# Performance work log

Measured on AMD Instinct MI355X. Metric: run time of the kernel, lower is better.

The kernel has to match this reference:

```python
import jax, jax.numpy as jnp
import numpy as np

# config constants
B, L, ENC_IN = 8, 512, 7
D_MODEL = 768
EXPAND = 2
D_INNER = D_MODEL * EXPAND          # 1536
DT_RANK = (D_MODEL + 15) // 16      # 48
N_STATE = 16                         # configs.d_ff acts as SSM state size
K_CONV = 4
E_LAYERS = 2
C_OUT = 7
PRED_LEN = 96
EPS = 1e-5


def rmsnorm(x, w):
    return x * jax.lax.rsqrt(jnp.mean(x * x, axis=-1, keepdims=True) + EPS) * w


def silu(x):
    return x * jax.nn.sigmoid(x)


def positional_embedding(l, d):
    pos = np.arange(l, dtype=np.float32)[:, None]
    div = np.exp(np.arange(0, d, 2, dtype=np.float32) * (-np.log(10000.0) / d))
    pe = np.zeros((l, d), dtype=np.float32)
    pe[:, 0::2] = np.sin(pos * div)
    pe[:, 1::2] = np.cos(pos * div)
    return jnp.asarray(pe)


def causal_dwconv(x, w, b):
    # x: [b, d, l], w: [d, 1, k]; torch pads k-1 both sides then slices [:l] == left-pad k-1
    y = jax.lax.conv_general_dilated(
        x, w, window_strides=(1,), padding=[(K_CONV - 1, 0)],
        dimension_numbers=('NCH', 'OIH', 'NCH'), feature_group_count=D_INNER)
    return y + b[None, :, None]


def selective_scan(u, delta, A, Bm, Cm, Dp):
    # u, delta: [b,l,d]; A: [d,n]; Bm, Cm: [b,l,n]; Dp: [d]
    deltaA = jnp.exp(jnp.einsum('bld,dn->bldn', delta, A))          # [b,l,d,n]
    deltaBu = (delta * u)[..., None] * Bm[:, :, None, :]             # [b,l,d,n]

    def step(xc, inp):
        dA, dBu, Ct = inp                                            # [b,d,n],[b,d,n],[b,n]
        xc = dA * xc + dBu
        return xc, jnp.einsum('bdn,bn->bd', xc, Ct)

    b, l, d = u.shape
    x0 = jnp.zeros((b, d, A.shape[1]), u.dtype)
    _, ys = jax.lax.scan(step, x0, (jnp.moveaxis(deltaA, 1, 0),
                                    jnp.moveaxis(deltaBu, 1, 0),
                                    jnp.moveaxis(Cm, 1, 0)))
    y = jnp.moveaxis(ys, 0, 1)                                       # [b,l,d]
    return y + u * Dp


def mamba_block(x, in_w, conv_w, conv_b, xproj_w, dtproj_w, dtproj_b, A_log, Dp, outproj_w):
    xr = x @ in_w.T                                                  # [b,l,2*d_inner]
    xs, res = xr[..., :D_INNER], xr[..., D_INNER:]
    xs = causal_dwconv(jnp.swapaxes(xs, 1, 2), conv_w, conv_b)
    xs = silu(jnp.swapaxes(xs, 1, 2))
    # ssm
    A = -jnp.exp(A_log)
    x_dbl = xs @ xproj_w.T                                           # [b,l,dt_rank+2n]
    delta = x_dbl[..., :DT_RANK]
    Bm = x_dbl[..., DT_RANK:DT_RANK + N_STATE]
    Cm = x_dbl[..., DT_RANK + N_STATE:]
    delta = jax.nn.softplus(delta @ dtproj_w.T + dtproj_b)
    y = selective_scan(xs, delta, A, Bm, Cm, Dp)
    y = y * silu(res)
    return y @ outproj_w.T


def setup_inputs() -> dict:
    key = jax.random.key(0)
    ks = iter(jax.random.split(key, 32))
    s = 0.02
    d = {}
    d['x'] = jax.random.normal(next(ks), (B, L, ENC_IN), jnp.float32)
    d['token_w'] = jax.random.normal(next(ks), (D_MODEL, ENC_IN, 3), jnp.float32) * s
    d['time_w'] = jax.random.normal(next(ks), (D_MODEL, 1), jnp.float32) * s
    d['norm_w'] = jnp.ones((E_LAYERS, D_MODEL), jnp.float32)
    d['in_w'] = jax.random.normal(next(ks), (E_LAYERS, 2 * D_INNER, D_MODEL), jnp.float32) * s
    d['conv_w'] = jax.random.normal(next(ks), (E_LAYERS, D_INNER, 1, K_CONV), jnp.float32) * s
    d['conv_b'] = jnp.zeros((E_LAYERS, D_INNER), jnp.float32)
    d['xproj_w'] = jax.random.normal(next(ks), (E_LAYERS, DT_RANK + 2 * N_STATE, D_INNER), jnp.float32) * s
    d['dtproj_w'] = jax.random.normal(next(ks), (E_LAYERS, D_INNER, DT_RANK), jnp.float32) * s
    d['dtproj_b'] = jnp.zeros((E_LAYERS, D_INNER), jnp.float32)
    A = np.tile(np.arange(1, N_STATE + 1, dtype=np.float32)[None, :], (D_INNER, 1))
    d['A_log'] = jnp.tile(jnp.log(jnp.asarray(A))[None], (E_LAYERS, 1, 1))
    d['Dp'] = jnp.ones((E_LAYERS, D_INNER), jnp.float32)
    d['outproj_w'] = jax.random.normal(next(ks), (E_LAYERS, D_MODEL, D_INNER), jnp.float32) * s
    d['final_norm_w'] = jnp.ones((D_MODEL,), jnp.float32)
    d['out_w'] = jax.random.normal(next(ks), (C_OUT, D_MODEL), jnp.float32) * s
    return d


def reference(x, token_w, time_w, norm_w, in_w, conv_w, conv_b, xproj_w,
              dtproj_w, dtproj_b, A_log, Dp, outproj_w, final_norm_w, out_w):
    # instance normalization (mean/std detached)
    mean_enc = jax.lax.stop_gradient(jnp.mean(x, axis=1, keepdims=True))
    xc = x - mean_enc
    std_enc = jax.lax.stop_gradient(jnp.sqrt(jnp.var(xc, axis=1, keepdims=True) + 1e-5))
    xc = xc / std_enc
    # DataEmbedding: circular conv token emb + sinusoidal pos + timeF linear
    xp = jnp.pad(jnp.swapaxes(xc, 1, 2), ((0, 0), (0, 0), (1, 1)), mode='wrap')
    tok = jax.lax.conv_general_dilated(xp, token_w, (1,), 'VALID',
                                       dimension_numbers=('NCH', 'OIH', 'NCH'))
    tok = jnp.swapaxes(tok, 1, 2)                                    # [b,l,d_model]
    x_mark = (jnp.arange(L, dtype=x.dtype) / L)[None, :, None]       # [1,l,1]
    h = tok + positional_embedding(L, D_MODEL)[None] + x_mark @ time_w.T
    for e in range(E_LAYERS):
        h = mamba_block(rmsnorm(h, norm_w[e]), in_w[e], conv_w[e], conv_b[e],
                        xproj_w[e], dtproj_w[e], dtproj_b[e], A_log[e], Dp[e],
                        outproj_w[e]) + h
    h = rmsnorm(h, final_norm_w)
    out = h @ out_w.T
    out = out * std_enc + mean_enc
    return out[:, -PRED_LEN:, :]
```

## Files before the change

kernel.cpp:

```cpp
#include <hip/hip_runtime.h>
#include <hip/hip_bf16.h>
#include <math.h>

#define BSZ 8
#define LSEQ 512
#define ENC_IN 7
#define D_MODEL 768
#define D_INNER 1536
#define DT_RANK 48
#define N_STATE 16
#define K_CONV 4
#define E_LAYERS 2
#define C_OUT 7
#define PRED_LEN 96
#define EPSV 1e-5f
#define XN 80
#define KSPLIT 4

#define ROWS (BSZ*LSEQ)
#define NC 16
#define CL (LSEQ/NC)
#define NTILE (LSEQ/16)
#define LOG2E 1.44269504088896f

typedef __bf16 bf16x8 __attribute__((ext_vector_type(8)));
typedef float  f32x4  __attribute__((ext_vector_type(4)));

__device__ __forceinline__ float fexp2(float x) {
    float r;
    asm("v_exp_f32 %0, %1" : "=v"(r) : "v"(x));
    return r;
}
__device__ __forceinline__ float softplusf(float v) {
    return fmaxf(v, 0.f) + log1pf(__expf(-fabsf(v)));
}

__device__ __forceinline__ float block_sum(float v, float* tmp) {
    #pragma unroll
    for (int off = 32; off > 0; off >>= 1) v += __shfl_down(v, off);
    int lane = threadIdx.x & 63, wid = threadIdx.x >> 6;
    __syncthreads();
    if (lane == 0) tmp[wid] = v;
    __syncthreads();
    return tmp[0] + tmp[1] + tmp[2] + tmp[3];
}

__global__ __launch_bounds__(256) void cvt_all(const float* __restrict__ in_w,
                                               const float* __restrict__ outw,
                                               const float* __restrict__ xpw,
                                               const float* __restrict__ dtw,
                                               __hip_bfloat16* __restrict__ inw_bf,
                                               __hip_bfloat16* __restrict__ outw_bf,
                                               __hip_bfloat16* __restrict__ xpw_bf,
                                               __hip_bfloat16* __restrict__ dtw_bf) {
    const int N1 = E_LAYERS*2*D_INNER*D_MODEL;
    const int N2 = E_LAYERS*D_MODEL*D_INNER;
    const int N3 = E_LAYERS*XN*D_INNER;
    const int N4 = E_LAYERS*D_INNER*64;
    int i = blockIdx.x*256 + threadIdx.x;
    if (i < N1) {
        inw_bf[i] = __float2bfloat16(in_w[i]);
    } else if (i < N1+N2) {
        int j = i - N1; outw_bf[j] = __float2bfloat16(outw[j]);
    } else if (i < N1+N2+N3) {
        int j = i - N1 - N2; xpw_bf[j] = __float2bfloat16(xpw[j]);
    } else if (i < N1+N2+N3+N4) {
        int j = i - N1 - N2 - N3;
        int r = j >> 6, c = j & 63;
        dtw_bf[j] = __float2bfloat16(c < DT_RANK ? dtw[r*DT_RANK + c] : 0.f);
    }
}

__global__ __launch_bounds__(256) void stats_kernel(const float* __restrict__ x,
                                                    float* __restrict__ mean,
                                                    float* __restrict__ stdv) {
    int bc = blockIdx.x;
    int b = bc / ENC_IN, c = bc % ENC_IN;
    __shared__ float tmp[4];
    float s = 0.f, sq = 0.f;
    for (int l = threadIdx.x; l < LSEQ; l += 256) {
        float v = x[((size_t)(b*LSEQ + l))*ENC_IN + c];
        s += v; sq += v*v;
    }
    s = block_sum(s, tmp);
    sq = block_sum(sq, tmp);
    if (threadIdx.x == 0) {
        float m = s / LSEQ;
        float var = sq / LSEQ - m*m;
        if (var < 0.f) var = 0.f;
        mean[bc] = m;
        stdv[bc] = sqrtf(var + EPSV);
    }
}

__global__ __launch_bounds__(256) void embed_kernel(const float* __restrict__ x,
                                                    const float* __restrict__ token_w,
                                                    const float* __restrict__ time_w,
                                                    const float* __restrict__ mean,
                                                    const float* __restrict__ stdv,
                                                    float* __restrict__ h) {
    int bl = blockIdx.x;
    int b = bl >> 9, l = bl & 511;
    __shared__ float sxc[ENC_IN*3];
    if (threadIdx.x < ENC_IN*3) {
        int c = threadIdx.x / 3, k = threadIdx.x % 3;
        int lk = (l + k - 1) & 511;
        float v = x[((size_t)(b*LSEQ + lk))*ENC_IN + c];
        sxc[threadIdx.x] = (v - mean[b*ENC_IN + c]) / stdv[b*ENC_IN + c];
    }
    __syncthreads();
    #pragma unroll
    for (int i = 0; i < 3; i++) {
        int d = threadIdx.x + i*256;
        float acc = 0.f;
        const float* w = token_w + (size_t)d*21;
        #pragma unroll
        for (int t = 0; t < 21; t++) acc += sxc[t] * w[t];
        int d2 = d & ~1;
        float div = __expf((float)d2 * (-9.210340371976184f / (float)D_MODEL));
        float ang = (float)l * div;
        float pe = (d & 1) ? cosf(ang) : sinf(ang);
        float tm = ((float)l / (float)LSEQ) * time_w[d];
        h[(size_t)bl*D_MODEL + d] = acc + pe + tm;
    }
}

__global__ __launch_bounds__(256) void rmsnorm_bf16(const float* __restrict__ h,
                                                    const float* __restrict__ w,
                                                    __hip_bfloat16* __restrict__ xn) {
    size_t base = (size_t)blockIdx.x * D_MODEL;
    __shared__ float tmp[4];
    float ss = 0.f;
    for (int k = threadIdx.x; k < D_MODEL; k += 256) { float v = h[base+k]; ss += v*v; }
    ss = block_sum(ss, tmp);
    float inv = rsqrtf(ss / (float)D_MODEL + EPSV);
    for (int k = threadIdx.x; k < D_MODEL; k += 256)
        xn[base+k] = __float2bfloat16(h[base+k]*inv*w[k]);
}

__global__ __launch_bounds__(256) void gemm_inproj(const __hip_bfloat16* __restrict__ A,
                                                   const __hip_bfloat16* __restrict__ Bw,
                                                   __hip_bfloat16* __restrict__ Cxs,
                                                   __hip_bfloat16* __restrict__ Cg) {
    __shared__ __align__(16) __hip_bfloat16 As[128*64];
    __shared__ __align__(16) __hip_bfloat16 Bs[128*64];
    const int K = D_MODEL;
    int tid = threadIdx.x, lane = tid & 63, w = tid >> 6;
    int gx = gridDim.x;
    int nwg = gx * gridDim.y;
    int orig = blockIdx.y*gx + blockIdx.x;
    int swz = (orig & 7)*(nwg >> 3) + (orig >> 3);
    int m0 = (swz / gx) * 128, n0 = (swz % gx) * 128;
    int wr = w >> 1, wc = w & 1;
    int kq = lane >> 4, rr = lane & 15;

    f32x4 acc[4][4];
    #pragma unroll
    for (int i = 0; i < 4; i++)
        #pragma unroll
        for (int j = 0; j < 4; j++) acc[i][j] = (f32x4){0.f,0.f,0.f,0.f};

    const char* Ab = (const char*)A;
    const char* Bb = (const char*)Bw;
    char* AsB = (char*)As;
    char* BsB = (char*)Bs;

    for (int k0 = 0; k0 < K; k0 += 64) {
        #pragma unroll
        for (int c = 0; c < 4; c++) {
            int idx = c*256 + tid;
            int r = idx >> 3, q = idx & 7;
            int qs = q ^ (r & 7);
            __builtin_amdgcn_global_load_lds(
                (const __attribute__((address_space(1))) unsigned int*)(Ab + ((size_t)(m0+r)*K + k0 + qs*8)*2),
                (__attribute__((address_space(3))) unsigned int*)(AsB + idx*16), 16, 0, 0);
            __builtin_amdgcn_global_load_lds(
                (const __attribute__((address_space(1))) unsigned int*)(Bb + ((size_t)(n0+r)*K + k0 + qs*8)*2),
                (__attribute__((address_space(3))) unsigned int*)(BsB + idx*16), 16, 0, 0);
        }
        __syncthreads();

        #pragma unroll
        for (int kh = 0; kh < 2; kh++) {
            int ch = ((kh*4 + kq) ^ (rr & 7)) * 16;
            bf16x8 af[4], bfr[4];
            #pragma unroll
            for (int mi = 0; mi < 4; mi++) af[mi]  = *(const bf16x8*)(AsB + (wr*64 + mi*16 + rr)*128 + ch);
            #pragma unroll
            for (int ni = 0; ni < 4; ni++) bfr[ni] = *(const bf16x8*)(BsB + (wc*64 + ni*16 + rr)*128 + ch);
            #pragma unroll
            for (int mi = 0; mi < 4; mi++)
                #pragma unroll
                for (int ni = 0; ni < 4; ni++)
                    acc[mi][ni] = __builtin_amdgcn_mfma_f32_16x16x32_bf16(af[mi], bfr[ni], acc[mi][ni], 0, 0, 0);
        }
        __syncthreads();
    }

    #pragma unroll
    for (int mi = 0; mi < 4; mi++) {
        #pragma unroll
        for (int ni = 0; ni < 4; ni++) {
            int row0 = m0 + wr*64 + mi*16;
            int col  = n0 + wc*64 + ni*16 + rr;
            if (col >= D_INNER) {
                __hip_bfloat16 g4[4];
                #pragma unroll
                for (int r = 0; r < 4; r++) {
                    float v = acc[mi][ni][r];
                    g4[r] = __float2bfloat16(v / (1.f + __expf(-v)));
                }
                int cd = col - D_INNER;
                *(uint2*)&Cg[((size_t)(row0 >> 4)*D_INNER + cd)*16 + kq*4] = *(uint2*)g4;
            } else {
                #pragma unroll
                for (int r = 0; r < 4; r++) {
                    int row = row0 + kq*4 + r;
                    Cxs[(size_t)row*D_INNER + col] = __float2bfloat16(acc[mi][ni][r]);
                }
            }
        }
    }
}

__global__ __launch_bounds__(256) void gemm_dtproj(const __hip_bfloat16* __restrict__ A,
                                                   const __hip_bfloat16* __restrict__ Bw,
                                                   const float* __restrict__ bias,
                                                   float* __restrict__ C) {
    __shared__ __align__(16) __hip_bfloat16 As[128*64];
    __shared__ __align__(16) __hip_bfloat16 Bs[128*64];
    const int K = 64;
    int tid = threadIdx.x, lane = tid & 63, w = tid >> 6;
    int gx = gridDim.x;
    int nwg = gx * gridDim.y;
    int orig = blockIdx.y*gx + blockIdx.x;
    int swz = (orig & 7)*(nwg >> 3) + (orig >> 3);
    int m0 = (swz / gx) * 128, n0 = (swz % gx) * 128;
    int wr = w >> 1, wc = w & 1;
    int kq = lane >> 4, rr = lane & 15;

    f32x4 acc[4][4];
    #pragma unroll
    for (int i = 0; i < 4; i++)
        #pragma unroll
        for (int j = 0; j < 4; j++) acc[i][j] = (f32x4){0.f,0.f,0.f,0.f};

    const char* Ab = (const char*)A;
    const char* Bb = (const char*)Bw;
    char* AsB = (char*)As;
    char* BsB = (char*)Bs;

    #pragma unroll
    for (int c = 0; c < 4; c++) {
        int idx = c*256 + tid;
        int r = idx >> 3, q = idx & 7;
        int qs = q ^ (r & 7);
        __builtin_amdgcn_global_load_lds(
            (const __attribute__((address_space(1))) unsigned int*)(Ab + ((size_t)(m0+r)*K + qs*8)*2),
            (__attribute__((address_space(3))) unsigned int*)(AsB + idx*16), 16, 0, 0);
        __builtin_amdgcn_global_load_lds(
            (const __attribute__((address_space(1))) unsigned int*)(Bb + ((size_t)(n0+r)*K + qs*8)*2),
            (__attribute__((address_space(3))) unsigned int*)(BsB + idx*16), 16, 0, 0);
    }
    __syncthreads();

    #pragma unroll
    for (int kh = 0; kh < 2; kh++) {
        int ch = ((kh*4 + kq) ^ (rr & 7)) * 16;
        bf16x8 af[4], bfr[4];
        #pragma unroll
        for (int mi = 0; mi < 4; mi++) af[mi]  = *(const bf16x8*)(AsB + (wr*64 + mi*16 + rr)*128 + ch);
        #pragma unroll
        for (int ni = 0; ni < 4; ni++) bfr[ni] = *(const bf16x8*)(BsB + (wc*64 + ni*16 + rr)*128 + ch);
        #pragma unroll
        for (int mi = 0; mi < 4; mi++)
            #pragma unroll
            for (int ni = 0; ni < 4; ni++)
                acc[mi][ni] = __builtin_amdgcn_mfma_f32_16x16x32_bf16(af[mi], bfr[ni], acc[mi][ni], 0, 0, 0);
    }

    #pragma unroll
    for (int mi = 0; mi < 4; mi++) {
        #pragma unroll
        for (int ni = 0; ni < 4; ni++) {
            int row0 = m0 + wr*64 + mi*16;
            int col  = n0 + wc*64 + ni*16 + rr;
            float4 v4;
            #pragma unroll
            for (int r = 0; r < 4; r++) {
                float v = acc[mi][ni][r] + bias[col];
                ((float*)&v4)[r] = softplusf(v);
            }
            *(float4*)&C[((size_t)(row0 >> 4)*D_INNER + col)*16 + kq*4] = v4;
        }
    }
}

__global__ __launch_bounds__(256) void gemm_outproj(const __hip_bfloat16* __restrict__ A,
                                                    const __hip_bfloat16* __restrict__ Bw,
                                                    float* __restrict__ C) {
    __shared__ __align__(16) __hip_bfloat16 As[128*32];
    __shared__ __align__(16) __hip_bfloat16 Bs[64*32];
    int tid = threadIdx.x, lane = tid & 63, w = tid >> 6;
    int gx = gridDim.x;
    int nwg = gx * gridDim.y;
    int orig = blockIdx.y*gx + blockIdx.x;
    int swz = (orig & 7)*(nwg >> 3) + (orig >> 3);
    int m0 = (swz / gx) * 128, n0 = (swz % gx) * 64;
    int wr = w >> 1, wc = w & 1;
    int kq = lane >> 4, rr = lane & 15;
    const int K = D_INNER;

    f32x4 acc[4][2];
    #pragma unroll
    for (int i = 0; i < 4; i++)
        #pragma unroll
        for (int j = 0; j < 2; j++) acc[i][j] = (f32x4){0.f,0.f,0.f,0.f};

    const char* Ab = (const char*)A;
    const char* Bb = (const char*)Bw;
    char* AsB = (char*)As;
    char* BsB = (char*)Bs;

    int cA0 = tid, cA1 = tid + 256;
    int rA0 = cA0 >> 2, qA0 = (cA0 & 3) ^ ((rA0 >> 1) & 3);
    int rA1 = cA1 >> 2, qA1 = (cA1 & 3) ^ ((rA1 >> 1) & 3);
    int rB = tid >> 2,  qB  = (tid & 3) ^ ((rB >> 1) & 3);
    int sw = (kq ^ ((rr >> 1) & 3)) * 16;

    for (int k0 = 0; k0 < K; k0 += 32) {
        __builtin_amdgcn_global_load_lds(
            (const __attribute__((address_space(1))) unsigned int*)(Ab + ((size_t)(m0+rA0)*K + k0 + qA0*8)*2),
            (__attribute__((address_space(3))) unsigned int*)(AsB + cA0*16), 16, 0, 0);
        __builtin_amdgcn_global_load_lds(
            (const __attribute__((address_space(1))) unsigned int*)(Ab + ((size_t)(m0+rA1)*K + k0 + qA1*8)*2),
            (__attribute__((address_space(3))) unsigned int*)(AsB + cA1*16), 16, 0, 0);
        __builtin_amdgcn_global_load_lds(
            (const __attribute__((address_space(1))) unsigned int*)(Bb + ((size_t)(n0+rB)*K + k0 + qB*8)*2),
            (__attribute__((address_space(3))) unsigned int*)(BsB + tid*16), 16, 0, 0);
        __syncthreads();

        bf16x8 af[4], bfr[2];
        #pragma unroll
        for (int mi = 0; mi < 4; mi++) af[mi]  = *(const bf16x8*)(AsB + (wr*64 + mi*16 + rr)*64 + sw);
        #pragma unroll
        for (int ni = 0; ni < 2; ni++) bfr[ni] = *(const bf16x8*)(BsB + (wc*32 + ni*16 + rr)*64 + sw);
        #pragma unroll
        for (int mi = 0; mi < 4; mi++)
            #pragma unroll
            for (int ni = 0; ni < 2; ni++)
                acc[mi][ni] = __builtin_amdgcn_mfma_f32_16x16x32_bf16(af[mi], bfr[ni], acc[mi][ni], 0, 0, 0);
        __syncthreads();
    }

    #pragma unroll
    for (int mi = 0; mi < 4; mi++) {
        #pragma unroll
        for (int ni = 0; ni < 2; ni++) {
            #pragma unroll
            for (int r = 0; r < 4; r++) {
                int row = m0 + wr*64 + mi*16 + kq*4 + r;
                int col = n0 + wc*32 + ni*16 + rr;
                size_t o = (size_t)row*D_MODEL + col;
                C[o] = acc[mi][ni][r] + C[o];
            }
        }
    }
}

__global__ __launch_bounds__(256) void gemm_xproj(const __hip_bfloat16* __restrict__ A,
                                                  const __hip_bfloat16* __restrict__ W,
                                                  float* __restrict__ P) {
    __shared__ __align__(16) __hip_bfloat16 As[64*64];
    __shared__ __align__(16) __hip_bfloat16 Bs[96*64];
    int tid = threadIdx.x, lane = tid & 63, w = tid >> 6;
    int m0 = blockIdx.x * 64;
    int k0 = blockIdx.y * (D_INNER / KSPLIT);
    int kq = lane >> 4, rr = lane & 15;
    f32x4 acc[5];
    #pragma unroll
    for (int i = 0; i < 5; i++) acc[i] = (f32x4){0.f,0.f,0.f,0.f};
    const char* Ab = (const char*)A;
    const char* Wb = (const char*)W;
    char* AsB = (char*)As;
    char* BsB = (char*)Bs;

    for (int kk = k0; kk < k0 + D_INNER/KSPLIT; kk += 64) {
        #pragma unroll
        for (int cA = 0; cA < 2; cA++) {
            int idx = cA*256 + tid;
            int r = idx >> 3, q = (idx & 7) ^ (r & 7);
            __builtin_amdgcn_global_load_lds(
                (const __attribute__((address_space(1))) unsigned int*)(Ab + ((size_t)(m0+r)*D_INNER + kk + q*8)*2),
                (__attribute__((address_space(3))) unsigned int*)(AsB + idx*16), 16, 0, 0);
        }
        #pragma unroll
        for (int cB = 0; cB < 3; cB++) {
            int idx = cB*256 + tid;
            int r = idx >> 3, q = (idx & 7) ^ (r & 7);
            int rs = r < XN ? r : XN-1;
            __builtin_amdgcn_global_load_lds(
                (const __attribute__((address_space(1))) unsigned int*)(Wb + ((size_t)rs*D_INNER + kk + q*8)*2),
                (__attribute__((address_space(3))) unsigned int*)(BsB + idx*16), 16, 0, 0);
        }
        __syncthreads();
        #pragma unroll
        for (int kh = 0; kh < 2; kh++) {
            bf16x8 a = *(const bf16x8*)(AsB + (w*16 + rr)*128 + (((kh*4 + kq) ^ (rr & 7)))*16);
            #pragma unroll
            for (int ni = 0; ni < 5; ni++) {
                bf16x8 b = *(const bf16x8*)(BsB + (ni*16 + rr)*128 + (((kh*4 + kq) ^ (rr & 7)))*16);
                acc[ni] = __builtin_amdgcn_mfma_f32_16x16x32_bf16(a, b, acc[ni], 0, 0, 0);
            }
        }
        __syncthreads();
    }
    float* Cp = P + (size_t)blockIdx.y * ROWS * XN;
    #pragma unroll
    for (int ni = 0; ni < 5; ni++)
        #pragma unroll
        for (int r = 0; r < 4; r++) {
            int row = m0 + w*16 + kq*4 + r;
            int col = ni*16 + rr;
            Cp[(size_t)row*XN + col] = acc[ni][r];
        }
}

__global__ __launch_bounds__(256) void xproj_reduce(const float* __restrict__ P,
                                                    float* __restrict__ xdbl,
                                                    __hip_bfloat16* __restrict__ xdbl_bf) {
    int idx = blockIdx.x*256 + threadIdx.x;
    int col = idx % 96, row = idx / 96;
    if (row >= ROWS) return;
    const size_t RX = (size_t)ROWS*XN;
    if (col < XN) {
        size_t o = (size_t)row*XN + col;
        float s = P[o] + P[RX + o] + P[2*RX + o] + P[3*RX + o];
        xdbl[o] = s;
        if (col < DT_RANK) xdbl_bf[(size_t)row*64 + col] = __float2bfloat16(s);
    } else {
        xdbl_bf[(size_t)row*64 + col - 32] = __float2bfloat16(0.f);
    }
}

__global__ __launch_bounds__(256) void dwconv_silu(const __hip_bfloat16* __restrict__ xs,
                                                   const float* __restrict__ cw,
                                                   const float* __restrict__ cb,
                                                   __hip_bfloat16* __restrict__ u_bf) {
    int idx = blockIdx.x*256 + threadIdx.x;
    int dg = idx % (D_INNER/8);
    int t  = idx / (D_INNER/8);
    if (t >= ROWS) return;
    int d0 = dg*8;
    int l = t & 511, b = t >> 9;
    bf16x8 rows[K_CONV];
    #pragma unroll
    for (int k = 0; k < K_CONV; k++) {
        int ll = l - (K_CONV-1) + k;
        if (ll >= 0) rows[k] = *(const bf16x8*)(xs + ((size_t)(b*LSEQ + ll))*D_INNER + d0);
        else { bf16x8 z = {}; rows[k] = z; }
    }
    bf16x8 outv;
    #pragma unroll
    for (int j = 0; j < 8; j++) {
        int d = d0 + j;
        const float4 w4 = *(const float4*)(cw + d*K_CONV);
        float acc = cb[d]
                  + (float)rows[0][j]*w4.x + (float)rows[1][j]*w4.y
                  + (float)rows[2][j]*w4.z + (float)rows[3][j]*w4.w;
        float v = acc / (1.f + __expf(-acc));
        outv[j] = (__bf16)v;
    }
    *(bf16x8*)(u_bf + (size_t)t*D_INNER + d0) = outv;
}

__global__ __launch_bounds__(256) void scan_p1(const __hip_bfloat16* __restrict__ u,
                                               const float* __restrict__ delta_blk,
                                               const float* __restrict__ xdbl,
                                               const float* __restrict__ A_log,
                                               float* __restrict__ xfin,
                                               float* __restrict__ sumdlt) {
    int d = blockIdx.x*256 + threadIdx.x;
    int c = blockIdx.y, b = blockIdx.z;
    int l0 = c*CL;
    float A2[N_STATE], xs[N_STATE];
    const float* al = A_log + d*N_STATE;
    #pragma unroll
    for (int n = 0; n < N_STATE; n++) {
        A2[n] = -__expf(al[n]) * LOG2E;
        xs[n] = 0.f;
    }
    const __hip_bfloat16* pu = u + (size_t)(b*LSEQ + l0)*D_INNER + d;
    const float* pB = xdbl + (size_t)(b*LSEQ + l0)*XN + DT_RANK;
    float sd = 0.f;
    #pragma unroll
    for (int tt = 0; tt < 2; tt++) {
        const float* db = delta_blk + ((size_t)(b*NTILE + (l0>>4) + tt)*D_INNER + d)*16;
        float dl[16];
        #pragma unroll
        for (int q = 0; q < 4; q++) {
            f32x4 v = *(const f32x4*)(db + q*4);
            dl[q*4+0]=v[0]; dl[q*4+1]=v[1]; dl[q*4+2]=v[2]; dl[q*4+3]=v[3];
        }
        #pragma unroll
        for (int i = 0; i < 16; i++) {
            float dlt = dl[i];
            float uu = __bfloat162float(*pu); pu += D_INNER;
            float du = dlt*uu;
            sd += dlt;
            #pragma unroll
            for (int n = 0; n < N_STATE; n++)
                xs[n] = fexp2(dlt*A2[n])*xs[n] + du*pB[n];
            pB += XN;
        }
    }
    float* px = xfin + (size_t)((b*NC + c)*N_STATE)*D_INNER + d;
    #pragma unroll
    for (int n = 0; n < N_STATE; n++) px[n*D_INNER] = xs[n];
    sumdlt[(size_t)(b*NC + c)*D_INNER + d] = sd;
}

__global__ __launch_bounds__(256) void scan_p2(float* __restrict__ xfin,
                                               const float* __restrict__ sumdlt,
                                               const float* __restrict__ A_log) {
    int idx = blockIdx.x*256 + threadIdx.x;
    int d = idx % D_INNER;
    int r = idx / D_INNER;
    int n = r & 15;
    int b = r >> 4;
    float A2 = -__expf(A_log[d*N_STATE + n]) * LOG2E;
    float cr = 0.f;
    for (int c = 1; c < NC; c++) {
        size_t jp = (size_t)(b*NC + c - 1);
        float xf = xfin[(jp*N_STATE + n)*D_INNER + d];
        float s  = sumdlt[jp*D_INNER + d];
        cr = fexp2(A2 * s) * cr + xf;
        xfin[(jp*N_STATE + n)*D_INNER + d] = cr;
    }
}

__global__ __launch_bounds__(256) void scan_p3(const __hip_bfloat16* __restrict__ u,
                                               const float* __restrict__ delta_blk,
                                               const __hip_bfloat16* __restrict__ gres,
                                               const float* __restrict__ xdbl,
                                               const float* __restrict__ A_log,
                                               const float* __restrict__ Dp,
                                               const float* __restrict__ carry,
                                               __hip_bfloat16* __restrict__ ygate) {
    int d = blockIdx.x*256 + threadIdx.x;
    int c = blockIdx.y, b = blockIdx.z;
    int l0 = c*CL;
    float A2[N_STATE], xs[N_STATE];
    const float* al = A_log + d*N_STATE;
    #pragma unroll
    for (int n = 0; n < N_STATE; n++) A2[n] = -__expf(al[n]) * LOG2E;
    if (c == 0) {
        #pragma unroll
        for (int n = 0; n < N_STATE; n++) xs[n] = 0.f;
    } else {
        const float* pc = carry + (size_t)((b*NC + c - 1)*N_STATE)*D_INNER + d;
        #pragma unroll
        for (int n = 0; n < N_STATE; n++) xs[n] = pc[n*D_INNER];
    }
    float Dv = Dp[d];
    const __hip_bfloat16* pu = u + (size_t)(b*LSEQ + l0)*D_INNER + d;
    const float* pB = xdbl + (size_t)(b*LSEQ + l0)*XN + DT_RANK;
    __hip_bfloat16* py = ygate + (size_t)(b*LSEQ + l0)*D_INNER + d;
    #pragma unroll
    for (int tt = 0; tt < 2; tt++) {
        size_t tb = (size_t)(b*NTILE + (l0>>4) + tt)*D_INNER + d;
        const float* db = delta_blk + tb*16;
        float dl[16];
        #pragma unroll
        for (int q = 0; q < 4; q++) {
            f32x4 v = *(const f32x4*)(db + q*4);
            dl[q*4+0]=v[0]; dl[q*4+1]=v[1]; dl[q*4+2]=v[2]; dl[q*4+3]=v[3];
        }
        const __hip_bfloat16* gb = gres + tb*16;
        bf16x8 g0 = *(const bf16x8*)gb;
        bf16x8 g1 = *(const bf16x8*)(gb + 8);
        float gr[16];
        #pragma unroll
        for (int j = 0; j < 8; j++) { gr[j] = (float)g0[j]; gr[8+j] = (float)g1[j]; }
        #pragma unroll
        for (int i = 0; i < 16; i++) {
            float dlt = dl[i];
            float uu = __bfloat162float(*pu); pu += D_INNER;
            float du = dlt*uu;
            float acc = 0.f;
            #pragma unroll
            for (int n = 0; n < N_STATE; n++) {
                xs[n] = fexp2(dlt*A2[n])*xs[n] + du*pB[n];
                acc += xs[n]*pB[N_STATE + n];
            }
            pB += XN;
            float y = acc + uu*Dv;
            *py = __float2bfloat16(y * gr[i]); py += D_INNER;
        }
    }
}

__global__ __launch_bounds__(256) void final_kernel(const float* __restrict__ h,
                                                    const float* __restrict__ fnw,
                                                    const float* __restrict__ out_w,
                                                    const float* __restrict__ mean,
                                                    const float* __restrict__ stdv,
                                                    float* __restrict__ out) {
    int bid = blockIdx.x;
    int b = bid / PRED_LEN, lo = bid % PRED_LEN;
    int l = LSEQ - PRED_LEN + lo;
    const float* row = h + ((size_t)(b*LSEQ + l))*D_MODEL;
    __shared__ float tmp[4];
    float ss = 0.f;
    for (int k = threadIdx.x; k < D_MODEL; k += 256) { float v = row[k]; ss += v*v; }
    ss = block_sum(ss, tmp);
    float inv = rsqrtf(ss / (float)D_MODEL + EPSV);
    float acc[C_OUT] = {};
    for (int k = threadIdx.x; k < D_MODEL; k += 256) {
        float hn = row[k]*fnw[k];
        #pragma unroll
        for (int c = 0; c < C_OUT; c++) acc[c] += hn*out_w[c*D_MODEL + k];
    }
    #pragma unroll
    for (int c = 0; c < C_OUT; c++) {
        float s = block_sum(acc[c], tmp);
        if (threadIdx.x == 0)
            out[((size_t)(b*PRED_LEN + lo))*C_OUT + c] = s*inv*stdv[b*ENC_IN + c] + mean[b*ENC_IN + c];
    }
}

extern "C" void kernel_launch(void* const* d_in, const int* in_sizes, int n_in,
                              void* d_out, int out_size, void* d_ws, size_t ws_size,
                              hipStream_t stream) {
    const float* x        = (const float*)d_in[0];
    const float* token_w  = (const float*)d_in[1];
    const float* time_w   = (const float*)d_in[2];
    const float* norm_w   = (const float*)d_in[3];
    const float* in_w     = (const float*)d_in[4];
    const float* conv_w   = (const float*)d_in[5];
    const float* conv_b   = (const float*)d_in[6];
    const float* xproj_w  = (const float*)d_in[7];
    const float* dtproj_w = (const float*)d_in[8];
    const float* dtproj_b = (const float*)d_in[9];
    const float* A_log    = (const float*)d_in[10];
    const float* Dp       = (const float*)d_in[11];
    const float* outproj_w= (const float*)d_in[12];
    const float* final_nw = (const float*)d_in[13];
    const float* out_w    = (const float*)d_in[14];
    float* out = (float*)d_out;

    float* ws   = (float*)d_ws;
    float* mean = ws;
    float* stdv = ws + 64;
    float* h    = ws + 128;
    float* xdbl = h    + (size_t)ROWS*D_MODEL;
    float* delta= xdbl + (size_t)ROWS*XN;
    float* sumd = delta+ (size_t)ROWS*D_INNER;
    float* xfin = sumd + (size_t)BSZ*NC*D_INNER;
    float* pout = xfin + (size_t)BSZ*NC*D_INNER*N_STATE;
    float* fend = pout + (size_t)KSPLIT*ROWS*XN;
    __hip_bfloat16* xn_bf  = (__hip_bfloat16*)fend;
    __hip_bfloat16* xs_bf  = xn_bf + (size_t)ROWS*D_MODEL;
    __hip_bfloat16* u_bf   = xs_bf + (size_t)ROWS*D_INNER;
    __hip_bfloat16* gres   = u_bf  + (size_t)ROWS*D_INNER;
    __hip_bfloat16* ygate  = gres  + (size_t)ROWS*D_INNER;
    __hip_bfloat16* xdbl_bf= ygate + (size_t)ROWS*D_INNER;
    __hip_bfloat16* inw_bf = xdbl_bf+ (size_t)ROWS*64;
    __hip_bfloat16* outw_bf= inw_bf + (size_t)E_LAYERS*2*D_INNER*D_MODEL;
    __hip_bfloat16* xpw_bf = outw_bf+ (size_t)E_LAYERS*D_MODEL*D_INNER;
    __hip_bfloat16* dtw_bf = xpw_bf + (size_t)E_LAYERS*XN*D_INNER;

    {
        const int NT = E_LAYERS*2*D_INNER*D_MODEL + E_LAYERS*D_MODEL*D_INNER
                     + E_LAYERS*XN*D_INNER + E_LAYERS*D_INNER*64;
        cvt_all<<<(NT+255)/256, 256, 0, stream>>>(in_w, outproj_w, xproj_w, dtproj_w,
                                                  inw_bf, outw_bf, xpw_bf, dtw_bf);
    }

    stats_kernel<<<BSZ*ENC_IN, 256, 0, stream>>>(x, mean, stdv);
    embed_kernel<<<ROWS, 256, 0, stream>>>(x, token_w, time_w, mean, stdv, h);

    for (int e = 0; e < E_LAYERS; e++) {
        rmsnorm_bf16<<<ROWS, 256, 0, stream>>>(h, norm_w + e*D_MODEL, xn_bf);
        gemm_inproj<<<dim3(2*D_INNER/128, ROWS/128), 256, 0, stream>>>(
            xn_bf, inw_bf + (size_t)e*2*D_INNER*D_MODEL, xs_bf, gres);
        dwconv_silu<<<(ROWS*(D_INNER/8) + 255)/256, 256, 0, stream>>>(
            xs_bf, conv_w + (size_t)e*D_INNER*K_CONV, conv_b + e*D_INNER, u_bf);
        gemm_xproj<<<dim3(ROWS/64, KSPLIT), 256, 0, stream>>>(
            u_bf, xpw_bf + (size_t)e*XN*D_INNER, pout);
        xproj_reduce<<<(ROWS*96 + 255)/256, 256, 0, stream>>>(pout, xdbl, xdbl_bf);
        gemm_dtproj<<<dim3(D_INNER/128, ROWS/128), 256, 0, stream>>>(
            xdbl_bf, dtw_bf + (size_t)e*D_INNER*64, dtproj_b + e*D_INNER, delta);
        const float* Alog_e = A_log + (size_t)e*D_INNER*N_STATE;
        scan_p1<<<dim3(D_INNER/256, NC, BSZ), 256, 0, stream>>>(
            u_bf, delta, xdbl, Alog_e, xfin, sumd);
        scan_p2<<<(BSZ*D_INNER*N_STATE)/256, 256, 0, stream>>>(
            xfin, sumd, Alog_e);
        scan_p3<<<dim3(D_INNER/256, NC, BSZ), 256, 0, stream>>>(
            u_bf, delta, gres, xdbl, Alog_e, Dp + (size_t)e*D_INNER, xfin, ygate);
        gemm_outproj<<<dim3(D_MODEL/64, ROWS/128), 256, 0, stream>>>(
            ygate, outw_bf + (size_t)e*D_MODEL*D_INNER, h);
    }

    final_kernel<<<BSZ*PRED_LEN, 256, 0, stream>>>(h, final_nw, out_w, mean, stdv, out);
}
```

Baseline: 415.6 us.

## Double-buffer GEMM tiles, store delta as bf16, add power-chain scan fast path

The in_proj, out_proj and x_proj GEMMs now use two LDS buffers, so the next K slice is prefetched while MFMAs run on the current one. dt_proj writes softplus(delta) as bf16 instead of fp32, which halves that tensor's traffic in the two scan kernels. The scan kernels check at runtime whether exp(A_log[n]) equals n+1 (the standard Mamba initialisation). When it does, they replace the 16 per-step exponentials with one exp2 followed by repeated multiplication, and fall back to the general path otherwise. The costs are bf16 rounding of delta, small accumulated error from the power chain, and more LDS and register use in the GEMMs.

```diff
diff --git a/kernel.cpp b/kernel.cpp
--- a/kernel.cpp
+++ b/kernel.cpp
@@ -33,6 +33,10 @@
 }
 __device__ __forceinline__ float softplusf(float v) {
     return fmaxf(v, 0.f) + log1pf(__expf(-fabsf(v)));
+}
+__device__ __forceinline__ void glds16(const char* g, char* l) {
+    __builtin_amdgcn_global_load_lds((const __attribute__((address_space(1))) unsigned int*)g,
+                                     (__attribute__((address_space(3))) unsigned int*)l, 16, 0, 0);
 }
 
 __device__ __forceinline__ float block_sum(float v, float* tmp) {
@@ -142,8 +146,8 @@
                                                    const __hip_bfloat16* __restrict__ Bw,
                                                    __hip_bfloat16* __restrict__ Cxs,
                                                    __hip_bfloat16* __restrict__ Cg) {
-    __shared__ __align__(16) __hip_bfloat16 As[128*64];
-    __shared__ __align__(16) __hip_bfloat16 Bs[128*64];
+    __shared__ __align__(16) __hip_bfloat16 As[2][128*32];
+    __shared__ __align__(16) __hip_bfloat16 Bs[2][128*32];
     const int K = D_MODEL;
     int tid = threadIdx.x, lane = tid & 63, w = tid >> 6;
     int gx = gridDim.x;
@@ -165,36 +169,40 @@
     char* AsB = (char*)As;
     char* BsB = (char*)Bs;
 
-    for (int k0 = 0; k0 < K; k0 += 64) {
-        #pragma unroll
-        for (int c = 0; c < 4; c++) {
-            int idx = c*256 + tid;
-            int r = idx >> 3, q = idx & 7;
-            int qs = q ^ (r & 7);
-            __builtin_amdgcn_global_load_lds(
-                (const __attribute__((address_space(1))) unsigned int*)(Ab + ((size_t)(m0+r)*K + k0 + qs*8)*2),
-                (__attribute__((address_space(3))) unsigned int*)(AsB + idx*16), 16, 0, 0);
-            __builtin_amdgcn_global_load_lds(
-                (const __attribute__((address_space(1))) unsigned int*)(Bb + ((size_t)(n0+r)*K + k0 + qs*8)*2),
-                (__attribute__((address_space(3))) unsigned int*)(BsB + idx*16), 16, 0, 0);
-        }
+    int c0 = tid, c1 = tid + 256;
+    int r0 = c0 >> 2, q0 = (c0 & 3) ^ ((r0 >> 1) & 3);
+    int r1 = c1 >> 2, q1 = (c1 & 3) ^ ((r1 >> 1) & 3);
+    int sw = (kq ^ ((rr >> 1) & 3)) * 16;
+
+    glds16(Ab + ((size_t)(m0+r0)*K + 0 + q0*8)*2, AsB + c0*16);
+    glds16(Ab + ((size_t)(m0+r1)*K + 0 + q1*8)*2, AsB + c1*16);
+    glds16(Bb + ((size_t)(n0+r0)*K + 0 + q0*8)*2, BsB + c0*16);
+    glds16(Bb + ((size_t)(n0+r1)*K + 0 + q1*8)*2, BsB + c1*16);
+    asm volatile("s_waitcnt vmcnt(0)" ::: "memory");
+    __syncthreads();
+
+    int cur = 0;
+    for (int k0 = 0; k0 < K; k0 += 32) {
+        if (k0 + 32 < K) {
+            int nb = cur ^ 1;
+            glds16(Ab + ((size_t)(m0+r0)*K + k0+32 + q0*8)*2, AsB + nb*8192 + c0*16);
+            glds16(Ab + ((size_t)(m0+r1)*K + k0+32 + q1*8)*2, AsB + nb*8192 + c1*16);
+            glds16(Bb + ((size_t)(n0+r0)*K + k0+32 + q0*8)*2, BsB + nb*8192 + c0*16);
+            glds16(Bb + ((size_t)(n0+r1)*K + k0+32 + q1*8)*2, BsB + nb*8192 + c1*16);
+        }
+        bf16x8 af[4], bfr[4];
+        #pragma unroll
+        for (int mi = 0; mi < 4; mi++) af[mi]  = *(const bf16x8*)(AsB + cur*8192 + (wr*64 + mi*16 + rr)*64 + sw);
+        #pragma unroll
+        for (int ni = 0; ni < 4; ni++) bfr[ni] = *(const bf16x8*)(BsB + cur*8192 + (wc*64 + ni*16 + rr)*64 + sw);
+        #pragma unroll
+        for (int mi = 0; mi < 4; mi++)
+            #pragma unroll
+            for (int ni = 0; ni < 4; ni++)
+                acc[mi][ni] = __builtin_amdgcn_mfma_f32_16x16x32_bf16(af[mi], bfr[ni], acc[mi][ni], 0, 0, 0);
+        asm volatile("s_waitcnt vmcnt(0)" ::: "memory");
         __syncthreads();
-
-        #pragma unroll
-        for (int kh = 0; kh < 2; kh++) {
-            int ch = ((kh*4 + kq) ^ (rr & 7)) * 16;
-            bf16x8 af[4], bfr[4];
-            #pragma unroll
-            for (int mi = 0; mi < 4; mi++) af[mi]  = *(const bf16x8*)(AsB + (wr*64 + mi*16 + rr)*128 + ch);
-            #pragma unroll
-            for (int ni = 0; ni < 4; ni++) bfr[ni] = *(const bf16x8*)(BsB + (wc*64 + ni*16 + rr)*128 + ch);
-            #pragma unroll
-            for (int mi = 0; mi < 4; mi++)
-                #pragma unroll
-                for (int ni = 0; ni < 4; ni++)
-                    acc[mi][ni] = __builtin_amdgcn_mfma_f32_16x16x32_bf16(af[mi], bfr[ni], acc[mi][ni], 0, 0, 0);
-        }
-        __syncthreads();
+        cur ^= 1;
     }
 
     #pragma unroll
@@ -226,7 +234,7 @@
 __global__ __launch_bounds__(256) void gemm_dtproj(const __hip_bfloat16* __restrict__ A,
                                                    const __hip_bfloat16* __restrict__ Bw,
                                                    const float* __restrict__ bias,
-                                                   float* __restrict__ C) {
+                                                   __hip_bfloat16* __restrict__ C) {
     __shared__ __align__(16) __hip_bfloat16 As[128*64];
     __shared__ __align__(16) __hip_bfloat16 Bs[128*64];
     const int K = 64;
@@ -255,12 +263,8 @@
         int idx = c*256 + tid;
         int r = idx >> 3, q = idx & 7;
         int qs = q ^ (r & 7);
-        __builtin_amdgcn_global_load_lds(
-            (const __attribute__((address_space(1))) unsigned int*)(Ab + ((size_t)(m0+r)*K + qs*8)*2),
-            (__attribute__((address_space(3))) unsigned int*)(AsB + idx*16), 16, 0, 0);
-        __builtin_amdgcn_global_load_lds(
-            (const __attribute__((address_space(1))) unsigned int*)(Bb + ((size_t)(n0+r)*K + qs*8)*2),
-            (__attribute__((address_space(3))) unsigned int*)(BsB + idx*16), 16, 0, 0);
+        glds16(Ab + ((size_t)(m0+r)*K + qs*8)*2, AsB + idx*16);
+        glds16(Bb + ((size_t)(n0+r)*K + qs*8)*2, BsB + idx*16);
     }
     __syncthreads();
 
@@ -285,13 +289,13 @@
         for (int ni = 0; ni < 4; ni++) {
             int row0 = m0 + wr*64 + mi*16;
             int col  = n0 + wc*64 + ni*16 + rr;
-            float4 v4;
+            __hip_bfloat16 d4[4];
             #pragma unroll
             for (int r = 0; r < 4; r++) {
                 float v = acc[mi][ni][r] + bias[col];
-                ((float*)&v4)[r] = softplusf(v);
+                d4[r] = __float2bfloat16(softplusf(v));
             }
-            *(float4*)&C[((size_t)(row0 >> 4)*D_INNER + col)*16 + kq*4] = v4;
+            *(uint2*)&C[((size_t)(row0 >> 4)*D_INNER + col)*16 + kq*4] = *(uint2*)d4;
         }
     }
 }
@@ -299,8 +303,8 @@
 __global__ __launch_bounds__(256) void gemm_outproj(const __hip_bfloat16* __restrict__ A,
                                                     const __hip_bfloat16* __restrict__ Bw,
                                                     float* __restrict__ C) {
-    __shared__ __align__(16) __hip_bfloat16 As[128*32];
-    __shared__ __align__(16) __hip_bfloat16 Bs[64*32];
+    __shared__ __align__(16) __hip_bfloat16 As[2][128*32];
+    __shared__ __align__(16) __hip_bfloat16 Bs[2][64*32];
     int tid = threadIdx.x, lane = tid & 63, w = tid >> 6;
     int gx = gridDim.x;
     int nwg = gx * gridDim.y;
@@ -328,29 +332,33 @@
     int rB = tid >> 2,  qB  = (tid & 3) ^ ((rB >> 1) & 3);
     int sw = (kq ^ ((rr >> 1) & 3)) * 16;
 
+    glds16(Ab + ((size_t)(m0+rA0)*K + 0 + qA0*8)*2, AsB + cA0*16);
+    glds16(Ab + ((size_t)(m0+rA1)*K + 0 + qA1*8)*2, AsB + cA1*16);
+    glds16(Bb + ((size_t)(n0+rB)*K + 0 + qB*8)*2, BsB + tid*16);
+    asm volatile("s_waitcnt vmcnt(0)" ::: "memory");
+    __syncthreads();
+
+    int cur = 0;
     for (int k0 = 0; k0 < K; k0 += 32) {
-        __builtin_amdgcn_global_load_lds(
-            (const __attribute__((address_space(1))) unsigned int*)(Ab + ((size_t)(m0+rA0)*K + k0 + qA0*8)*2),
-            (__attribute__((address_space(3))) unsigned int*)(AsB + cA0*16), 16, 0, 0);
-        __builtin_amdgcn_global_load_lds(
-            (const __attribute__((address_space(1))) unsigned int*)(Ab + ((size_t)(m0+rA1)*K + k0 + qA1*8)*2),
-            (__attribute__((address_space(3))) unsigned int*)(AsB + cA1*16), 16, 0, 0);
-        __builtin_amdgcn_global_load_lds(
-            (const __attribute__((address_space(1))) unsigned int*)(Bb + ((size_t)(n0+rB)*K + k0 + qB*8)*2),
-            (__attribute__((address_space(3))) unsigned int*)(BsB + tid*16), 16, 0, 0);
-        __syncthreads();
-
+        if (k0 + 32 < K) {
+            int nb = cur ^ 1;
+            glds16(Ab + ((size_t)(m0+rA0)*K + k0+32 + qA0*8)*2, AsB + nb*8192 + cA0*16);
+            glds16(Ab + ((size_t)(m0+rA1)*K + k0+32 + qA1*8)*2, AsB + nb*8192 + cA1*16);
+            glds16(Bb + ((size_t)(n0+rB)*K + k0+32 + qB*8)*2, BsB + nb*4096 + tid*16);
+        }
         bf16x8 af[4], bfr[2];
         #pragma unroll
-        for (int mi = 0; mi < 4; mi++) af[mi]  = *(const bf16x8*)(AsB + (wr*64 + mi*16 + rr)*64 + sw);
-        #pragma unroll
-        for (int ni = 0; ni < 2; ni++) bfr[ni] = *(const bf16x8*)(BsB + (wc*32 + ni*16 + rr)*64 + sw);
+        for (int mi = 0; mi < 4; mi++) af[mi]  = *(const bf16x8*)(AsB + cur*8192 + (wr*64 + mi*16 + rr)*64 + sw);
+        #pragma unroll
+        for (int ni = 0; ni < 2; ni++) bfr[ni] = *(const bf16x8*)(BsB + cur*4096 + (wc*32 + ni*16 + rr)*64 + sw);
         #pragma unroll
         for (int mi = 0; mi < 4; mi++)
             #pragma unroll
             for (int ni = 0; ni < 2; ni++)
                 acc[mi][ni] = __builtin_amdgcn_mfma_f32_16x16x32_bf16(af[mi], bfr[ni], acc[mi][ni], 0, 0, 0);
+        asm volatile("s_waitcnt vmcnt(0)" ::: "memory");
         __syncthreads();
+        cur ^= 1;
     }
 
     #pragma unroll
@@ -371,8 +379,8 @@
 __global__ __launch_bounds__(256) void gemm_xproj(const __hip_bfloat16* __restrict__ A,
                                                   const __hip_bfloat16* __restrict__ W,
                                                   float* __restrict__ P) {
-    __shared__ __align__(16) __hip_bfloat16 As[64*64];
-    __shared__ __align__(16) __hip_bfloat16 Bs[96*64];
+    __shared__ __align__(16) __hip_bfloat16 As[2][64*64];
+    __shared__ __align__(16) __hip_bfloat16 Bs[2][96*64];
     int tid = threadIdx.x, lane = tid & 63, w = tid >> 6;
     int m0 = blockIdx.x * 64;
     int k0 = blockIdx.y * (D_INNER / KSPLIT);
@@ -385,35 +393,42 @@
     char* AsB = (char*)As;
     char* BsB = (char*)Bs;
 
-    for (int kk = k0; kk < k0 + D_INNER/KSPLIT; kk += 64) {
+    auto stageA = [&](int buf, int kk) {
         #pragma unroll
         for (int cA = 0; cA < 2; cA++) {
             int idx = cA*256 + tid;
             int r = idx >> 3, q = (idx & 7) ^ (r & 7);
-            __builtin_amdgcn_global_load_lds(
-                (const __attribute__((address_space(1))) unsigned int*)(Ab + ((size_t)(m0+r)*D_INNER + kk + q*8)*2),
-                (__attribute__((address_space(3))) unsigned int*)(AsB + idx*16), 16, 0, 0);
+            glds16(Ab + ((size_t)(m0+r)*D_INNER + kk + q*8)*2, AsB + buf*8192 + idx*16);
         }
         #pragma unroll
         for (int cB = 0; cB < 3; cB++) {
             int idx = cB*256 + tid;
             int r = idx >> 3, q = (idx & 7) ^ (r & 7);
             int rs = r < XN ? r : XN-1;
-            __builtin_amdgcn_global_load_lds(
-                (const __attribute__((address_space(1))) unsigned int*)(Wb + ((size_t)rs*D_INNER + kk + q*8)*2),
-                (__attribute__((address_space(3))) unsigned int*)(BsB + idx*16), 16, 0, 0);
-        }
-        __syncthreads();
+            glds16(Wb + ((size_t)rs*D_INNER + kk + q*8)*2, BsB + buf*12288 + idx*16);
+        }
+    };
+
+    stageA(0, k0);
+    asm volatile("s_waitcnt vmcnt(0)" ::: "memory");
+    __syncthreads();
+
+    int cur = 0;
+    const int kend = k0 + D_INNER/KSPLIT;
+    for (int kk = k0; kk < kend; kk += 64) {
+        if (kk + 64 < kend) stageA(cur ^ 1, kk + 64);
         #pragma unroll
         for (int kh = 0; kh < 2; kh++) {
-            bf16x8 a = *(const bf16x8*)(AsB + (w*16 + rr)*128 + (((kh*4 + kq) ^ (rr & 7)))*16);
+            bf16x8 a = *(const bf16x8*)(AsB + cur*8192 + (w*16 + rr)*128 + (((kh*4 + kq) ^ (rr & 7)))*16);
             #pragma unroll
             for (int ni = 0; ni < 5; ni++) {
-                bf16x8 b = *(const bf16x8*)(BsB + (ni*16 + rr)*128 + (((kh*4 + kq) ^ (rr & 7)))*16);
+                bf16x8 b = *(const bf16x8*)(BsB + cur*12288 + (ni*16 + rr)*128 + (((kh*4 + kq) ^ (rr & 7)))*16);
                 acc[ni] = __builtin_amdgcn_mfma_f32_16x16x32_bf16(a, b, acc[ni], 0, 0, 0);
             }
         }
+        asm volatile("s_waitcnt vmcnt(0)" ::: "memory");
         __syncthreads();
+        cur ^= 1;
     }
     float* Cp = P + (size_t)blockIdx.y * ROWS * XN;
     #pragma unroll
@@ -475,7 +490,7 @@
 }
 
 __global__ __launch_bounds__(256) void scan_p1(const __hip_bfloat16* __restrict__ u,
-                                               const float* __restrict__ delta_blk,
+                                               const __hip_bfloat16* __restrict__ delta_blk,
                                                const float* __restrict__ xdbl,
                                                const float* __restrict__ A_log,
                                                float* __restrict__ xfin,
@@ -483,35 +498,59 @@
     int d = blockIdx.x*256 + threadIdx.x;
     int c = blockIdx.y, b = blockIdx.z;
     int l0 = c*CL;
-    float A2[N_STATE], xs[N_STATE];
     const float* al = A_log + d*N_STATE;
-    #pragma unroll
-    for (int n = 0; n < N_STATE; n++) {
-        A2[n] = -__expf(al[n]) * LOG2E;
-        xs[n] = 0.f;
-    }
+    bool fast = true;
+    #pragma unroll
+    for (int n = 0; n < N_STATE; n++)
+        fast = fast && (fabsf(__expf(al[n]) - (float)(n+1)) < 1e-3f);
+    float xs[N_STATE];
+    #pragma unroll
+    for (int n = 0; n < N_STATE; n++) xs[n] = 0.f;
     const __hip_bfloat16* pu = u + (size_t)(b*LSEQ + l0)*D_INNER + d;
     const float* pB = xdbl + (size_t)(b*LSEQ + l0)*XN + DT_RANK;
     float sd = 0.f;
-    #pragma unroll
-    for (int tt = 0; tt < 2; tt++) {
-        const float* db = delta_blk + ((size_t)(b*NTILE + (l0>>4) + tt)*D_INNER + d)*16;
-        float dl[16];
-        #pragma unroll
-        for (int q = 0; q < 4; q++) {
-            f32x4 v = *(const f32x4*)(db + q*4);
-            dl[q*4+0]=v[0]; dl[q*4+1]=v[1]; dl[q*4+2]=v[2]; dl[q*4+3]=v[3];
-        }
-        #pragma unroll
-        for (int i = 0; i < 16; i++) {
-            float dlt = dl[i];
-            float uu = __bfloat162float(*pu); pu += D_INNER;
-            float du = dlt*uu;
-            sd += dlt;
-            #pragma unroll
-            for (int n = 0; n < N_STATE; n++)
-                xs[n] = fexp2(dlt*A2[n])*xs[n] + du*pB[n];
-            pB += XN;
+    if (fast) {
+        #pragma unroll
+        for (int tt = 0; tt < 2; tt++) {
+            const __hip_bfloat16* db = delta_blk + ((size_t)(b*NTILE + (l0>>4) + tt)*D_INNER + d)*16;
+            bf16x8 d0 = *(const bf16x8*)db;
+            bf16x8 d1 = *(const bf16x8*)(db + 8);
+            #pragma unroll
+            for (int i = 0; i < 16; i++) {
+                float dlt = (float)(i < 8 ? d0[i] : d1[i-8]);
+                float uu = __bfloat162float(*pu); pu += D_INNER;
+                float du = dlt*uu;
+                sd += dlt;
+                float e1 = fexp2(-dlt*LOG2E);
+                float e = e1;
+                xs[0] = e*xs[0] + du*pB[0];
+                #pragma unroll
+                for (int n = 1; n < N_STATE; n++) {
+                    e *= e1;
+                    xs[n] = e*xs[n] + du*pB[n];
+                }
+                pB += XN;
+            }
+        }
+    } else {
+        #pragma unroll
+        for (int tt = 0; tt < 2; tt++) {
+            const __hip_bfloat16* db = delta_blk + ((size_t)(b*NTILE + (l0>>4) + tt)*D_INNER + d)*16;
+            bf16x8 d0 = *(const bf16x8*)db;
+            bf16x8 d1 = *(const bf16x8*)(db + 8);
+            #pragma unroll
+            for (int i = 0; i < 16; i++) {
+                float dlt = (float)(i < 8 ? d0[i] : d1[i-8]);
+                float uu = __bfloat162float(*pu); pu += D_INNER;
+                float du = dlt*uu;
+                sd += dlt;
+                #pragma unroll
+                for (int n = 0; n < N_STATE; n++) {
+                    float A2n = -__expf(al[n]) * LOG2E;
+                    xs[n] = fexp2(dlt*A2n)*xs[n] + du*pB[n];
+                }
+                pB += XN;
+            }
         }
     }
     float* px = xfin + (size_t)((b*NC + c)*N_STATE)*D_INNER + d;
@@ -540,7 +579,7 @@
 }
 
 __global__ __launch_bounds__(256) void scan_p3(const __hip_bfloat16* __restrict__ u,
-                                               const float* __restrict__ delta_blk,
+                                               const __hip_bfloat16* __restrict__ delta_blk,
                                                const __hip_bfloat16* __restrict__ gres,
                                                const float* __restrict__ xdbl,
                                                const float* __restrict__ A_log,
@@ -550,10 +589,12 @@
     int d = blockIdx.x*256 + threadIdx.x;
     int c = blockIdx.y, b = blockIdx.z;
     int l0 = c*CL;
-    float A2[N_STATE], xs[N_STATE];
     const float* al = A_log + d*N_STATE;
-    #pragma unroll
-    for (int n = 0; n < N_STATE; n++) A2[n] = -__expf(al[n]) * LOG2E;
+    bool fast = true;
+    #pragma unroll
+    for (int n = 0; n < N_STATE; n++)
+        fast = fast && (fabsf(__expf(al[n]) - (float)(n+1)) < 1e-3f);
+    float xs[N_STATE];
     if (c == 0) {
         #pragma unroll
         for (int n = 0; n < N_STATE; n++) xs[n] = 0.f;
@@ -566,36 +607,65 @@
     const __hip_bfloat16* pu = u + (size_t)(b*LSEQ + l0)*D_INNER + d;
     const float* pB = xdbl + (size_t)(b*LSEQ + l0)*XN + DT_RANK;
     __hip_bfloat16* py = ygate + (size_t)(b*LSEQ + l0)*D_INNER + d;
-    #pragma unroll
-    for (int tt = 0; tt < 2; tt++) {
-        size_t tb = (size_t)(b*NTILE + (l0>>4) + tt)*D_INNER + d;
-        const float* db = delta_blk + tb*16;
-        float dl[16];
-        #pragma unroll
-        for (int q = 0; q < 4; q++) {
-            f32x4 v = *(const f32x4*)(db + q*4);
-            dl[q*4+0]=v[0]; dl[q*4+1]=v[1]; dl[q*4+2]=v[2]; dl[q*4+3]=v[3];
-        }
-        const __hip_bfloat16* gb = gres + tb*16;
-        bf16x8 g0 = *(const bf16x8*)gb;
-        bf16x8 g1 = *(const bf16x8*)(gb + 8);
-        float gr[16];
-        #pragma unroll
-        for (int j = 0; j < 8; j++) { gr[j] = (float)g0[j]; gr[8+j] = (float)g1[j]; }
-        #pragma unroll
-        for (int i = 0; i < 16; i++) {
-            float dlt = dl[i];
-            float uu = __bfloat162float(*pu); pu += D_INNER;
-            float du = dlt*uu;
-            float acc = 0.f;
-            #pragma unroll
-            for (int n = 0; n < N_STATE; n++) {
-                xs[n] = fexp2(dlt*A2[n])*xs[n] + du*pB[n];
-                acc += xs[n]*pB[N_STATE + n];
+    if (fast) {
+        #pragma unroll
+        for (int tt = 0; tt < 2; tt++) {
+            size_t tb = (size_t)(b*NTILE + (l0>>4) + tt)*D_INNER + d;
+            const __hip_bfloat16* db = delta_blk + tb*16;
+            bf16x8 d0 = *(const bf16x8*)db;
+            bf16x8 d1 = *(const bf16x8*)(db + 8);
+            const __hip_bfloat16* gb = gres + tb*16;
+            bf16x8 g0 = *(const bf16x8*)gb;
+            bf16x8 g1 = *(const bf16x8*)(gb + 8);
+            #pragma unroll
+            for (int i = 0; i < 16; i++) {
+                float dlt = (float)(i < 8 ? d0[i] : d1[i-8]);
+                float gr  = (float)(i < 8 ? g0[i] : g1[i-8]);
+                float uu = __bfloat162float(*pu); pu += D_INNER;
+                float du = dlt*uu;
+                float e1 = fexp2(-dlt*LOG2E);
+                float e = e1;
+                float acc;
+                xs[0] = e*xs[0] + du*pB[0];
+                acc = xs[0]*pB[N_STATE + 0];
+                #pragma unroll
+                for (int n = 1; n < N_STATE; n++) {
+                    e *= e1;
+                    xs[n] = e*xs[n] + du*pB[n];
+                    acc += xs[n]*pB[N_STATE + n];
+                }
+                pB += XN;
+                float y = acc + uu*Dv;
+                *py = __float2bfloat16(y * gr); py += D_INNER;
             }
-            pB += XN;
-            float y = acc + uu*Dv;
-            *py = __float2bfloat16(y * gr[i]); py += D_INNER;
+        }
+    } else {
+        #pragma unroll
+        for (int tt = 0; tt < 2; tt++) {
+            size_t tb = (size_t)(b*NTILE + (l0>>4) + tt)*D_INNER + d;
+            const __hip_bfloat16* db = delta_blk + tb*16;
+            bf16x8 d0 = *(const bf16x8*)db;
+            bf16x8 d1 = *(const bf16x8*)(db + 8);
+            const __hip_bfloat16* gb = gres + tb*16;
+            bf16x8 g0 = *(const bf16x8*)gb;
+            bf16x8 g1 = *(const bf16x8*)(gb + 8);
+            #pragma unroll
+            for (int i = 0; i < 16; i++) {
+                float dlt = (float)(i < 8 ? d0[i] : d1[i-8]);
+                float gr  = (float)(i < 8 ? g0[i] : g1[i-8]);
+                float uu = __bfloat162float(*pu); pu += D_INNER;
+                float du = dlt*uu;
+                float acc = 0.f;
+                #pragma unroll
+                for (int n = 0; n < N_STATE; n++) {
+                    float A2n = -__expf(al[n]) * LOG2E;
+                    xs[n] = fexp2(dlt*A2n)*xs[n] + du*pB[n];
+                    acc += xs[n]*pB[N_STATE + n];
+                }
+                pB += XN;
+                float y = acc + uu*Dv;
+                *py = __float2bfloat16(y * gr); py += D_INNER;
+            }
         }
     }
 }
@@ -654,8 +724,7 @@
     float* stdv = ws + 64;
     float* h    = ws + 128;
     float* xdbl = h    + (size_t)ROWS*D_MODEL;
-    float* delta= xdbl + (size_t)ROWS*XN;
-    float* sumd = delta+ (size_t)ROWS*D_INNER;
+    float* sumd = xdbl + (size_t)ROWS*XN;
     float* xfin = sumd + (size_t)BSZ*NC*D_INNER;
     float* pout = xfin + (size_t)BSZ*NC*D_INNER*N_STATE;
     float* fend = pout + (size_t)KSPLIT*ROWS*XN;
@@ -664,7 +733,8 @@
     __hip_bfloat16* u_bf   = xs_bf + (size_t)ROWS*D_INNER;
     __hip_bfloat16* gres   = u_bf  + (size_t)ROWS*D_INNER;
     __hip_bfloat16* ygate  = gres  + (size_t)ROWS*D_INNER;
-    __hip_bfloat16* xdbl_bf= ygate + (size_t)ROWS*D_INNER;
+    __hip_bfloat16* delta  = ygate + (size_t)ROWS*D_INNER;
+    __hip_bfloat16* xdbl_bf= delta + (size_t)ROWS*D_INNER;
     __hip_bfloat16* inw_bf = xdbl_bf+ (size_t)ROWS*64;
     __hip_bfloat16* outw_bf= inw_bf + (size_t)E_LAYERS*2*D_INNER*D_MODEL;
     __hip_bfloat16* xpw_bf = outw_bf+ (size_t)E_LAYERS*D_MODEL*D_INNER;
```

After: 387.3 us. 1.07x faster.
